# Kernel optimization log

Measured on AMD Instinct MI355X. Metric: run time of the kernel, lower is better.

The kernel has to match this reference:

```python
import jax, jax.numpy as jnp
import numpy as np

B, K, C, O, I = 32, 1024, 64, 32, 32  # batch, num_capsules, num_classes, out_dim, in_dim
NUM_ROUTING = 3


def squash(x, axis=-1):
    sq = jnp.sum(x * x, axis=axis, keepdims=True)
    return (sq / (1.0 + sq)) * x / jnp.sqrt(sq + 1e-8)


def setup_inputs() -> dict:
    key = jax.random.key(0)
    kx, kw = jax.random.split(key)
    x = jax.random.normal(kx, (B, K, I), dtype=jnp.float32)
    W = jax.random.normal(kw, (K, C, O, I), dtype=jnp.float32) * 0.01
    return {"x": x, "W": W}


def reference(x, W):
    # u_hat[b,k,c,o] = sum_i W[k,c,o,i] * x[b,k,i]  (the torch repeat+matmul)
    u_hat = jnp.einsum('kcoi,bki->bkco', W, x)  # [B,K,C,O]
    b_ij = jnp.zeros((B, K, C, 1), dtype=x.dtype)
    c_ij = None
    v_j = None
    for i in range(NUM_ROUTING):
        c_ij = jax.nn.softmax(b_ij, axis=2)              # softmax over classes
        s_j = jnp.sum(c_ij * u_hat, axis=1, keepdims=True)  # [B,1,C,O]
        v_j = squash(s_j, axis=-1)
        if i < NUM_ROUTING - 1:
            agreement = jnp.sum(u_hat * v_j, axis=-1, keepdims=True)  # [B,K,C,1]
            b_ij = b_ij + agreement
    return v_j[:, 0], c_ij[..., 0]  # ([B,C,O], [B,K,C])
```

## Files before the change

### kernel.cpp

```cpp
#include <hip/hip_runtime.h>
#include <stdint.h>

#define Bb 32
#define Kk 1024
#define Cc 64
#define Oo 32
#define Ii 32

typedef __attribute__((ext_vector_type(8))) short bf16x8;
typedef __attribute__((ext_vector_type(4))) float f32x4;

__device__ __forceinline__ short f2bf(float f) {
    uint32_t u = __builtin_bit_cast(uint32_t, f);
    u += 0x7fffu + ((u >> 16) & 1u);
    return (short)(u >> 16);
}
__device__ __forceinline__ float bflo(uint32_t u) { return __builtin_bit_cast(float, u << 16); }
__device__ __forceinline__ float bfhi(uint32_t u) { return __builtin_bit_cast(float, u & 0xffff0000u); }
__device__ __forceinline__ uint32_t pk2(float a, float b) {
    return (uint32_t)(uint16_t)f2bf(a) | ((uint32_t)(uint16_t)f2bf(b) << 16);
}


__global__ __launch_bounds__(256) void k_uhat(const float* __restrict__ x,
                                              const float* __restrict__ W,
                                              uint16_t* __restrict__ uh) {
    const int k = blockIdx.x;
    const int lane = threadIdx.x & 63;
    const int wave = threadIdx.x >> 6;
    const int m = lane & 15;
    const int q = lane >> 4;

    bf16x8 bfrag[2];
#pragma unroll
    for (int nb = 0; nb < 2; ++nb) {
        const float* xp = x + (size_t)((nb * 16 + m) * Kk + k) * Ii + q * 8;
        f32x4 a = *(const f32x4*)xp;
        f32x4 b = *(const f32x4*)(xp + 4);
        bf16x8 t;
        t[0] = f2bf(a.x); t[1] = f2bf(a.y); t[2] = f2bf(a.z); t[3] = f2bf(a.w);
        t[4] = f2bf(b.x); t[5] = f2bf(b.y); t[6] = f2bf(b.z); t[7] = f2bf(b.w);
        bfrag[nb] = t;
    }

    for (int cc = 0; cc < 16; ++cc) {
        const int c = wave * 16 + cc;
        bf16x8 afrag[2];
#pragma unroll
        for (int mo = 0; mo < 2; ++mo) {
            const float* wp = W + (size_t)((k * Cc + c) * Oo + mo * 16 + m) * Ii + q * 8;
            f32x4 a = *(const f32x4*)wp;
            f32x4 b = *(const f32x4*)(wp + 4);
            bf16x8 t;
            t[0] = f2bf(a.x); t[1] = f2bf(a.y); t[2] = f2bf(a.z); t[3] = f2bf(a.w);
            t[4] = f2bf(b.x); t[5] = f2bf(b.y); t[6] = f2bf(b.z); t[7] = f2bf(b.w);
            afrag[mo] = t;
        }
        const f32x4 z = {0.f, 0.f, 0.f, 0.f};
        f32x4 d0 = __builtin_amdgcn_mfma_f32_16x16x32_bf16(afrag[0], bfrag[0], z, 0, 0, 0);
        f32x4 d1 = __builtin_amdgcn_mfma_f32_16x16x32_bf16(afrag[0], bfrag[1], z, 0, 0, 0);
        f32x4 d2 = __builtin_amdgcn_mfma_f32_16x16x32_bf16(afrag[1], bfrag[0], z, 0, 0, 0);
        f32x4 d3 = __builtin_amdgcn_mfma_f32_16x16x32_bf16(afrag[1], bfrag[1], z, 0, 0, 0);

        uint4 p0, p1;
        p0.x = pk2(d0.x, d0.y); p0.y = pk2(d0.z, d0.w);
        p0.z = pk2(d1.x, d1.y); p0.w = pk2(d1.z, d1.w);
        p1.x = pk2(d2.x, d2.y); p1.y = pk2(d2.z, d2.w);
        p1.z = pk2(d3.x, d3.y); p1.w = pk2(d3.z, d3.w);
        uint16_t* dst = uh + ((size_t)(k * Cc + c) * 64 + lane) * 16;
        *(uint4*)dst = p0;
        *(uint4*)(dst + 8) = p1;
    }
}

template <bool UNIFORM>
__global__ __launch_bounds__(256) void k_sacc(const uint16_t* __restrict__ uh,
                                              const float* __restrict__ cij,
                                              float* __restrict__ s) {
    const int lane = threadIdx.x & 63;
    const int wave = threadIdx.x >> 6;
    const int m = lane & 15;
    const int q = lane >> 4;
    const int c = (blockIdx.x & 15) * 4 + wave;
    const int k0 = (blockIdx.x >> 4) * 32;

    float acc[16];
#pragma unroll
    for (int i = 0; i < 16; ++i) acc[i] = 0.f;

    for (int kl = 0; kl < 32; ++kl) {
        const int k = k0 + kl;
        const uint16_t* up = uh + ((size_t)(k * Cc + c) * 64 + lane) * 16;
        uint4 q0 = *(const uint4*)up;
        uint4 q1 = *(const uint4*)(up + 8);
        float w0, w1;
        if (UNIFORM) {
            w0 = w1 = 1.0f / 64.0f;
        } else {
            const float* cp = cij + (size_t)(k * Cc + c) * Bb + m;
            w0 = cp[0];
            w1 = cp[16];
        }
        acc[0]  += w0 * bflo(q0.x);  acc[1]  += w0 * bfhi(q0.x);
        acc[2]  += w0 * bflo(q0.y);  acc[3]  += w0 * bfhi(q0.y);
        acc[4]  += w1 * bflo(q0.z);  acc[5]  += w1 * bfhi(q0.z);
        acc[6]  += w1 * bflo(q0.w);  acc[7]  += w1 * bfhi(q0.w);
        acc[8]  += w0 * bflo(q1.x);  acc[9]  += w0 * bfhi(q1.x);
        acc[10] += w0 * bflo(q1.y);  acc[11] += w0 * bfhi(q1.y);
        acc[12] += w1 * bflo(q1.z);  acc[13] += w1 * bfhi(q1.z);
        acc[14] += w1 * bflo(q1.w);  acc[15] += w1 * bfhi(q1.w);
    }
#pragma unroll
    for (int t = 0; t < 4; ++t) {
#pragma unroll
        for (int r = 0; r < 4; ++r) {
            const int b = (t & 1) * 16 + m;
            const int o = (t >> 1) * 16 + q * 4 + r;
            atomicAdd(&s[(size_t)(b * Cc + c) * Oo + o], acc[t * 4 + r]);
        }
    }
}

template <bool FIRST>
__global__ __launch_bounds__(256) void k_route(const uint16_t* __restrict__ uh,
                                               const float* __restrict__ v,
                                               float* __restrict__ bbuf,
                                               float* __restrict__ cbuf,
                                               float* __restrict__ outc) {
    __shared__ float agr[4 * 64 * 32];
    const int tid = threadIdx.x;
    const int lane = tid & 63;
    const int wave = tid >> 6;
    const int m = lane & 15;
    const int q = lane >> 4;
    const int k0 = blockIdx.x * 4;

    for (int cc = 0; cc < 16; ++cc) {
        const int c = wave * 16 + cc;
        f32x4 vv[4];
#pragma unroll
        for (int t = 0; t < 4; ++t) {
            const int b = (t & 1) * 16 + m;
            const int o = (t >> 1) * 16 + q * 4;
            vv[t] = *(const f32x4*)&v[(size_t)(b * Cc + c) * Oo + o];
        }
#pragma unroll
        for (int kl = 0; kl < 4; ++kl) {
            const int k = k0 + kl;
            const uint16_t* up = uh + ((size_t)(k * Cc + c) * 64 + lane) * 16;
            uint4 q0 = *(const uint4*)up;
            uint4 q1 = *(const uint4*)(up + 8);
            float p0 = bflo(q0.x) * vv[0].x + bfhi(q0.x) * vv[0].y
                     + bflo(q0.y) * vv[0].z + bfhi(q0.y) * vv[0].w
                     + bflo(q1.x) * vv[2].x + bfhi(q1.x) * vv[2].y
                     + bflo(q1.y) * vv[2].z + bfhi(q1.y) * vv[2].w;
            float p1 = bflo(q0.z) * vv[1].x + bfhi(q0.z) * vv[1].y
                     + bflo(q0.w) * vv[1].z + bfhi(q0.w) * vv[1].w
                     + bflo(q1.z) * vv[3].x + bfhi(q1.z) * vv[3].y
                     + bflo(q1.w) * vv[3].z + bfhi(q1.w) * vv[3].w;
            p0 += __shfl_xor(p0, 16);
            p0 += __shfl_xor(p0, 32);
            p1 += __shfl_xor(p1, 16);
            p1 += __shfl_xor(p1, 32);
            if (q == 0) {
                agr[(kl * 64 + c) * 32 + m] = p0;
                agr[(kl * 64 + c) * 32 + 16 + m] = p1;
            }
        }
    }
    __syncthreads();

    if (tid < 128) {
        const int kl = tid >> 5;
        const int b = tid & 31;
        const int k = k0 + kl;
        float row[64];
#pragma unroll
        for (int c = 0; c < 64; ++c) row[c] = agr[(kl * 64 + c) * 32 + b];
        if (FIRST) {
            float* bp = bbuf + (size_t)(k * Bb + b) * Cc;
#pragma unroll
            for (int c = 0; c < 64; ++c) bp[c] = row[c];
        } else {
            const float* bp = bbuf + (size_t)(k * Bb + b) * Cc;
#pragma unroll
            for (int c = 0; c < 64; ++c) row[c] += bp[c];
        }
        float mx = row[0];
#pragma unroll
        for (int c = 1; c < 64; ++c) mx = fmaxf(mx, row[c]);
        float sum = 0.f;
#pragma unroll
        for (int c = 0; c < 64; ++c) { row[c] = __expf(row[c] - mx); sum += row[c]; }
        const float inv = 1.f / sum;
#pragma unroll
        for (int c = 0; c < 64; ++c) row[c] *= inv;
        if (!FIRST) {
            float* op = outc + (size_t)(b * Kk + k) * Cc;
#pragma unroll
            for (int c = 0; c < 64; ++c) op[c] = row[c];
        }
#pragma unroll
        for (int c = 0; c < 64; ++c) agr[(kl * 64 + c) * 32 + b] = row[c];
    }
    __syncthreads();

    for (int idx = tid; idx < 4 * 64 * 32; idx += 256) {
        const int kl = idx >> 11;
        const int rem = idx & 2047;
        const int c = rem >> 5;
        const int b = rem & 31;
        cbuf[((size_t)(k0 + kl) * Cc + c) * Bb + b] = agr[idx];
    }
}

__global__ __launch_bounds__(256) void k_squash(const float* __restrict__ s,
                                                float* __restrict__ v) {
    const int row = blockIdx.x * 8 + (threadIdx.x >> 5);
    const int o = threadIdx.x & 31;
    float val = s[(size_t)row * 32 + o];
    float sq = val * val;
    sq += __shfl_xor(sq, 1);
    sq += __shfl_xor(sq, 2);
    sq += __shfl_xor(sq, 4);
    sq += __shfl_xor(sq, 8);
    sq += __shfl_xor(sq, 16);
    const float coef = sq / ((1.f + sq) * sqrtf(sq + 1e-8f));
    v[(size_t)row * 32 + o] = val * coef;
}

extern "C" void kernel_launch(void* const* d_in, const int* in_sizes, int n_in,
                              void* d_out, int out_size, void* d_ws, size_t ws_size,
                              hipStream_t stream) {
    (void)in_sizes; (void)n_in; (void)out_size;
    const float* x = (const float*)d_in[0];
    const float* W = (const float*)d_in[1];
    float* out_v = (float*)d_out;
    float* out_c = out_v + Bb * Cc * Oo;

    char* ws = (char*)d_ws;
    const size_t UH_BYTES = (size_t)Kk * Cc * 1024 * 2;
    const size_t BB_BYTES = (size_t)Kk * Bb * Cc * 4;
    const size_t SV = (size_t)Bb * Cc * Oo;

    uint16_t* uh = (uint16_t*)ws;
    float* bbuf = (float*)(ws + UH_BYTES);
    float* cbuf = (float*)(ws + UH_BYTES + BB_BYTES);
    float* s0 = (float*)(ws + UH_BYTES + 2 * BB_BYTES);
    float* s1 = s0 + SV;
    float* s2 = s1 + SV;
    float* v0 = s2 + SV;
    float* v1 = v0 + SV;
    const size_t NEED = UH_BYTES + 2 * BB_BYTES + 5 * SV * 4;
    if (ws_size < NEED) return;

    hipMemsetAsync(s0, 0, 3 * SV * 4, stream);

    k_uhat<<<Kk, 256, 0, stream>>>(x, W, uh);
    k_sacc<true><<<512, 256, 0, stream>>>(uh, nullptr, s0);
    k_squash<<<256, 256, 0, stream>>>(s0, v0);
    k_route<true><<<256, 256, 0, stream>>>(uh, v0, bbuf, cbuf, nullptr);
    k_sacc<false><<<512, 256, 0, stream>>>(uh, cbuf, s1);
    k_squash<<<256, 256, 0, stream>>>(s1, v1);
    k_route<false><<<256, 256, 0, stream>>>(uh, v1, bbuf, cbuf, out_c);
    k_sacc<false><<<512, 256, 0, stream>>>(uh, cbuf, s2);
    k_squash<<<256, 256, 0, stream>>>(s2, out_v);
}
```

Measured before the change: 598.4 us.

## Replace atomic s accumulation with partials plus fused reduce-squash and coalesced u_hat layout

k_sacc now writes per-chunk partial sums to a workspace buffer instead of issuing float atomicAdds. A new k_reduce kernel sums those partials, applies squash in registers, and writes v in the MFMA fragment layout that k_route reads directly. This removes the memset and the separate squash kernels. The u_hat storage is also reorganized so each wave's two 16-byte loads are contiguous across lanes, and W is read with nontemporal loads. The cost is an extra partials round trip through memory and a reduce kernel with only 64 blocks.

Measured after the change: 519.0 us. 13.3% less time.

```diff
diff --git a/kernel.cpp b/kernel.cpp
--- a/kernel.cpp
+++ b/kernel.cpp
@@ -24,7 +24,7 @@
 
 __global__ __launch_bounds__(256) void k_uhat(const float* __restrict__ x,
                                               const float* __restrict__ W,
-                                              uint16_t* __restrict__ uh) {
+                                              uint32_t* __restrict__ uh) {
     const int k = blockIdx.x;
     const int lane = threadIdx.x & 63;
     const int wave = threadIdx.x >> 6;
@@ -49,8 +49,8 @@
 #pragma unroll
         for (int mo = 0; mo < 2; ++mo) {
             const float* wp = W + (size_t)((k * Cc + c) * Oo + mo * 16 + m) * Ii + q * 8;
-            f32x4 a = *(const f32x4*)wp;
-            f32x4 b = *(const f32x4*)(wp + 4);
+            f32x4 a = __builtin_nontemporal_load((const f32x4*)wp);
+            f32x4 b = __builtin_nontemporal_load((const f32x4*)(wp + 4));
             bf16x8 t;
             t[0] = f2bf(a.x); t[1] = f2bf(a.y); t[2] = f2bf(a.z); t[3] = f2bf(a.w);
             t[4] = f2bf(b.x); t[5] = f2bf(b.y); t[6] = f2bf(b.z); t[7] = f2bf(b.w);
@@ -67,22 +67,22 @@
         p0.z = pk2(d1.x, d1.y); p0.w = pk2(d1.z, d1.w);
         p1.x = pk2(d2.x, d2.y); p1.y = pk2(d2.z, d2.w);
         p1.z = pk2(d3.x, d3.y); p1.w = pk2(d3.z, d3.w);
-        uint16_t* dst = uh + ((size_t)(k * Cc + c) * 64 + lane) * 16;
+        uint32_t* dst = uh + (size_t)(k * Cc + c) * 512 + lane * 4;
         *(uint4*)dst = p0;
-        *(uint4*)(dst + 8) = p1;
+        *(uint4*)(dst + 256) = p1;
     }
 }
 
 template <bool UNIFORM>
-__global__ __launch_bounds__(256) void k_sacc(const uint16_t* __restrict__ uh,
+__global__ __launch_bounds__(256) void k_sacc(const uint32_t* __restrict__ uh,
                                               const float* __restrict__ cij,
-                                              float* __restrict__ s) {
+                                              float* __restrict__ part) {
     const int lane = threadIdx.x & 63;
     const int wave = threadIdx.x >> 6;
     const int m = lane & 15;
-    const int q = lane >> 4;
     const int c = (blockIdx.x & 15) * 4 + wave;
-    const int k0 = (blockIdx.x >> 4) * 32;
+    const int chunk = blockIdx.x >> 4;
+    const int k0 = chunk * 32;
 
     float acc[16];
 #pragma unroll
@@ -90,9 +90,9 @@
 
     for (int kl = 0; kl < 32; ++kl) {
         const int k = k0 + kl;
-        const uint16_t* up = uh + ((size_t)(k * Cc + c) * 64 + lane) * 16;
+        const uint32_t* up = uh + (size_t)(k * Cc + c) * 512 + lane * 4;
         uint4 q0 = *(const uint4*)up;
-        uint4 q1 = *(const uint4*)(up + 8);
+        uint4 q1 = *(const uint4*)(up + 256);
         float w0, w1;
         if (UNIFORM) {
             w0 = w1 = 1.0f / 64.0f;
@@ -112,18 +112,81 @@
     }
 #pragma unroll
     for (int t = 0; t < 4; ++t) {
+        f32x4 v = {acc[t * 4 + 0], acc[t * 4 + 1], acc[t * 4 + 2], acc[t * 4 + 3]};
+        *(f32x4*)&part[(((size_t)(chunk * Cc + c) * 4 + t) * 64 + lane) * 4] = v;
+    }
+}
+
+template <bool FINAL>
+__global__ __launch_bounds__(256) void k_reduce(const float* __restrict__ part,
+                                                float* __restrict__ vfrag,
+                                                float* __restrict__ out_v) {
+    __shared__ float red[4 * 64 * 17];
+    const int c = blockIdx.x;
+    const int tid = threadIdx.x;
+    const int lane = tid & 63;
+    const int cg = tid >> 6;
+
+    float acc[16];
+#pragma unroll
+    for (int i = 0; i < 16; ++i) acc[i] = 0.f;
+    for (int ch = cg * 8; ch < cg * 8 + 8; ++ch) {
+        const f32x4* p = (const f32x4*)part + (size_t)(ch * Cc + c) * 4 * 64 + lane;
+#pragma unroll
+        for (int t = 0; t < 4; ++t) {
+            f32x4 v = p[t * 64];
+            acc[t * 4 + 0] += v.x; acc[t * 4 + 1] += v.y;
+            acc[t * 4 + 2] += v.z; acc[t * 4 + 3] += v.w;
+        }
+    }
+#pragma unroll
+    for (int i = 0; i < 16; ++i) red[(cg * 64 + lane) * 17 + i] = acc[i];
+    __syncthreads();
+
+    if (tid < 64) {
+        float a[16];
+#pragma unroll
+        for (int i = 0; i < 16; ++i)
+            a[i] = red[tid * 17 + i] + red[(64 + tid) * 17 + i]
+                 + red[(128 + tid) * 17 + i] + red[(192 + tid) * 17 + i];
+        float sq0 = 0.f, sq1 = 0.f;
 #pragma unroll
         for (int r = 0; r < 4; ++r) {
-            const int b = (t & 1) * 16 + m;
-            const int o = (t >> 1) * 16 + q * 4 + r;
-            atomicAdd(&s[(size_t)(b * Cc + c) * Oo + o], acc[t * 4 + r]);
+            sq0 += a[r] * a[r] + a[8 + r] * a[8 + r];
+            sq1 += a[4 + r] * a[4 + r] + a[12 + r] * a[12 + r];
+        }
+        sq0 += __shfl_xor(sq0, 16); sq0 += __shfl_xor(sq0, 32);
+        sq1 += __shfl_xor(sq1, 16); sq1 += __shfl_xor(sq1, 32);
+        const float c0 = sq0 / ((1.f + sq0) * sqrtf(sq0 + 1e-8f));
+        const float c1 = sq1 / ((1.f + sq1) * sqrtf(sq1 + 1e-8f));
+#pragma unroll
+        for (int r = 0; r < 4; ++r) {
+            a[r] *= c0; a[8 + r] *= c0;
+            a[4 + r] *= c1; a[12 + r] *= c1;
+        }
+        float* vp = vfrag + ((size_t)c * 64 + tid) * 16;
+#pragma unroll
+        for (int t = 0; t < 4; ++t) {
+            f32x4 v = {a[t * 4 + 0], a[t * 4 + 1], a[t * 4 + 2], a[t * 4 + 3]};
+            *(f32x4*)(vp + t * 4) = v;
+        }
+        if (FINAL) {
+            const int m = tid & 15, q = tid >> 4;
+#pragma unroll
+            for (int t = 0; t < 4; ++t)
+#pragma unroll
+                for (int r = 0; r < 4; ++r) {
+                    const int b = (t & 1) * 16 + m;
+                    const int o = (t >> 1) * 16 + q * 4 + r;
+                    out_v[((size_t)b * Cc + c) * Oo + o] = a[t * 4 + r];
+                }
         }
     }
 }
 
 template <bool FIRST>
-__global__ __launch_bounds__(256) void k_route(const uint16_t* __restrict__ uh,
-                                               const float* __restrict__ v,
+__global__ __launch_bounds__(256) void k_route(const uint32_t* __restrict__ uh,
+                                               const float* __restrict__ vfrag,
                                                float* __restrict__ bbuf,
                                                float* __restrict__ cbuf,
                                                float* __restrict__ outc) {
@@ -137,19 +200,16 @@
 
     for (int cc = 0; cc < 16; ++cc) {
         const int c = wave * 16 + cc;
+        const float* vp = vfrag + ((size_t)c * 64 + lane) * 16;
         f32x4 vv[4];
 #pragma unroll
-        for (int t = 0; t < 4; ++t) {
-            const int b = (t & 1) * 16 + m;
-            const int o = (t >> 1) * 16 + q * 4;
-            vv[t] = *(const f32x4*)&v[(size_t)(b * Cc + c) * Oo + o];
-        }
+        for (int t = 0; t < 4; ++t) vv[t] = *(const f32x4*)(vp + t * 4);
 #pragma unroll
         for (int kl = 0; kl < 4; ++kl) {
             const int k = k0 + kl;
-            const uint16_t* up = uh + ((size_t)(k * Cc + c) * 64 + lane) * 16;
+            const uint32_t* up = uh + (size_t)(k * Cc + c) * 512 + lane * 4;
             uint4 q0 = *(const uint4*)up;
-            uint4 q1 = *(const uint4*)(up + 8);
+            uint4 q1 = *(const uint4*)(up + 256);
             float p0 = bflo(q0.x) * vv[0].x + bfhi(q0.x) * vv[0].y
                      + bflo(q0.y) * vv[0].z + bfhi(q0.y) * vv[0].w
                      + bflo(q1.x) * vv[2].x + bfhi(q1.x) * vv[2].y
@@ -214,21 +274,6 @@
     }
 }
 
-__global__ __launch_bounds__(256) void k_squash(const float* __restrict__ s,
-                                                float* __restrict__ v) {
-    const int row = blockIdx.x * 8 + (threadIdx.x >> 5);
-    const int o = threadIdx.x & 31;
-    float val = s[(size_t)row * 32 + o];
-    float sq = val * val;
-    sq += __shfl_xor(sq, 1);
-    sq += __shfl_xor(sq, 2);
-    sq += __shfl_xor(sq, 4);
-    sq += __shfl_xor(sq, 8);
-    sq += __shfl_xor(sq, 16);
-    const float coef = sq / ((1.f + sq) * sqrtf(sq + 1e-8f));
-    v[(size_t)row * 32 + o] = val * coef;
-}
-
 extern "C" void kernel_launch(void* const* d_in, const int* in_sizes, int n_in,
                               void* d_out, int out_size, void* d_ws, size_t ws_size,
                               hipStream_t stream) {
@@ -239,30 +284,26 @@
     float* out_c = out_v + Bb * Cc * Oo;
 
     char* ws = (char*)d_ws;
-    const size_t UH_BYTES = (size_t)Kk * Cc * 1024 * 2;
+    const size_t UH_BYTES = (size_t)Kk * Cc * 512 * 4;
+    const size_t PART_BYTES = (size_t)32 * Cc * 4 * 64 * 4 * 4;
     const size_t BB_BYTES = (size_t)Kk * Bb * Cc * 4;
-    const size_t SV = (size_t)Bb * Cc * Oo;
-
-    uint16_t* uh = (uint16_t*)ws;
-    float* bbuf = (float*)(ws + UH_BYTES);
-    float* cbuf = (float*)(ws + UH_BYTES + BB_BYTES);
-    float* s0 = (float*)(ws + UH_BYTES + 2 * BB_BYTES);
-    float* s1 = s0 + SV;
-    float* s2 = s1 + SV;
-    float* v0 = s2 + SV;
-    float* v1 = v0 + SV;
-    const size_t NEED = UH_BYTES + 2 * BB_BYTES + 5 * SV * 4;
+    const size_t VF_BYTES = (size_t)Cc * 64 * 16 * 4;
+
+    uint32_t* uh = (uint32_t*)ws;
+    float* part  = (float*)(ws + UH_BYTES);
+    float* bbuf  = (float*)(ws + UH_BYTES + PART_BYTES);
+    float* cbuf  = (float*)(ws + UH_BYTES + PART_BYTES + BB_BYTES);
+    float* vfrag = (float*)(ws + UH_BYTES + PART_BYTES + 2 * BB_BYTES);
+    const size_t NEED = UH_BYTES + PART_BYTES + 2 * BB_BYTES + VF_BYTES;
     if (ws_size < NEED) return;
 
-    hipMemsetAsync(s0, 0, 3 * SV * 4, stream);
-
     k_uhat<<<Kk, 256, 0, stream>>>(x, W, uh);
-    k_sacc<true><<<512, 256, 0, stream>>>(uh, nullptr, s0);
-    k_squash<<<256, 256, 0, stream>>>(s0, v0);
-    k_route<true><<<256, 256, 0, stream>>>(uh, v0, bbuf, cbuf, nullptr);
-    k_sacc<false><<<512, 256, 0, stream>>>(uh, cbuf, s1);
-    k_squash<<<256, 256, 0, stream>>>(s1, v1);
-    k_route<false><<<256, 256, 0, stream>>>(uh, v1, bbuf, cbuf, out_c);
-    k_sacc<false><<<512, 256, 0, stream>>>(uh, cbuf, s2);
-    k_squash<<<256, 256, 0, stream>>>(s2, out_v);
-}
+    k_sacc<true><<<512, 256, 0, stream>>>(uh, nullptr, part);
+    k_reduce<false><<<Cc, 256, 0, stream>>>(part, vfrag, nullptr);
+    k_route<true><<<256, 256, 0, stream>>>(uh, vfrag, bbuf, cbuf, nullptr);
+    k_sacc<false><<<512, 256, 0, stream>>>(uh, cbuf, part);
+    k_reduce<false><<<Cc, 256, 0, stream>>>(part, vfrag, nullptr);
+    k_route<false><<<256, 256, 0, stream>>>(uh, vfrag, bbuf, cbuf, out_c);
+    k_sacc<false><<<512, 256, 0, stream>>>(uh, cbuf, part);
+    k_reduce<true><<<Cc, 256, 0, stream>>>(part, vfrag, out_v);
+}
```
